# Kernel optimization log

Hardware: AMD Instinct MI355X
Metric: run time of the kernel (lower is better)

## Reference

```python
import jax, jax.numpy as jnp
import numpy as np

EMBED_DIM = 768
NUM_HEADS = 12
HEAD_DIM = EMBED_DIM // NUM_HEADS
SCALE = HEAD_DIM ** -0.5


def setup_inputs() -> dict:
    key = jax.random.key(0)
    ks = jax.random.split(key, 9)
    B, S, D = 2, 2048, EMBED_DIM
    init = 1.0 / np.sqrt(D)  # ~ nn.Linear default uniform scale
    x = jax.random.normal(ks[0], (B, S, D), dtype=jnp.float32)
    Wq = jax.random.uniform(ks[1], (D, D), jnp.float32, -init, init)
    bq = jax.random.uniform(ks[2], (D,), jnp.float32, -init, init)
    Wk = jax.random.uniform(ks[3], (D, D), jnp.float32, -init, init)
    bk = jax.random.uniform(ks[4], (D,), jnp.float32, -init, init)
    Wv = jax.random.uniform(ks[5], (D, D), jnp.float32, -init, init)
    bv = jax.random.uniform(ks[6], (D,), jnp.float32, -init, init)
    Wo = jax.random.uniform(ks[7], (D, D), jnp.float32, -init, init)
    bo = jax.random.uniform(ks[8], (D,), jnp.float32, -init, init)
    return {"x": x, "Wq": Wq, "bq": bq, "Wk": Wk, "bk": bk,
            "Wv": Wv, "bv": bv, "Wo": Wo, "bo": bo}


def reference(x, Wq, bq, Wk, bk, Wv, bv, Wo, bo):
    B, S, D = x.shape
    H, Dh = NUM_HEADS, HEAD_DIM
    # projections; weights stored as (in, out) so x @ W == torch Linear with W.T
    q = (x @ Wq + bq).reshape(B, S, H, Dh).transpose(0, 2, 1, 3)  # [B,H,S,Dh]
    k = (x @ Wk + bk).reshape(B, S, H, Dh).transpose(0, 2, 1, 3)
    v = (x @ Wv + bv).reshape(B, S, H, Dh).transpose(0, 2, 1, 3)
    scores = jnp.einsum("bhqd,bhkd->bhqk", q, k) * SCALE        # [B,H,S,S]
    weights = jax.nn.softmax(scores, axis=-1)
    out = jnp.einsum("bhqk,bhkd->bhqd", weights, v)              # [B,H,S,Dh]
    out = out.transpose(0, 2, 1, 3).reshape(B, S, D)
    return out @ Wo + bo
```

## Files before the change

kernel.cpp:

```cpp
#include <hip/hip_runtime.h>
#include <math.h>

#define BB 2
#define SS 2048
#define DDIM 768
#define HH 12
#define DH 64
#define NROWS (BB*SS)
#define NQT2 (SS/128)

typedef _Float16 f16;
typedef _Float16 half2v __attribute__((ext_vector_type(2)));
typedef __fp16 fp16x2 __attribute__((ext_vector_type(2)));
typedef _Float16 half4 __attribute__((ext_vector_type(4)));
typedef _Float16 half8 __attribute__((ext_vector_type(8)));
typedef float f32x4 __attribute__((ext_vector_type(4)));
typedef float f32x16 __attribute__((ext_vector_type(16)));
typedef unsigned int u32;
typedef unsigned int u32x4v __attribute__((ext_vector_type(4)));

__device__ __forceinline__ half2v cvt_pk_f16(float a, float b) {
    fp16x2 t = __builtin_amdgcn_cvt_pkrtz(a, b);
    return __builtin_bit_cast(half2v, t);
}

#define MFMA16(a,b,c) __builtin_amdgcn_mfma_f32_16x16x32_f16((a),(b),(c),0,0,0)
#define MFMA32(a,b,c) __builtin_amdgcn_mfma_f32_32x32x16_f16((a),(b),(c),0,0,0)
#define QSCALE (0.125f * 1.44269504088896f)
#define M_STATIC 10.0f

__device__ __forceinline__ int swz(int row, int chunk16) {
    return row*128 + ((chunk16 ^ (row & 7)) << 4);
}

__global__ __launch_bounds__(256) void prep_w(const float* __restrict__ Wq, const float* __restrict__ Wk,
                                              const float* __restrict__ Wv, const float* __restrict__ Wo,
                                              f16* __restrict__ Wt)
{
    const int z = blockIdx.z;
    const float* W = z==0 ? Wq : (z==1 ? Wk : (z==2 ? Wv : Wo));
    f16* out = Wt + (size_t)z * DDIM * DDIM;

    __shared__ float tile[64][65];
    const int t = threadIdx.x;
    const int k0 = blockIdx.x*64, n0 = blockIdx.y*64;

    const int kr = t >> 2, nc = (t & 3) * 16;
    #pragma unroll
    for (int i = 0; i < 4; ++i) {
        float4 v = *(const float4*)&W[(size_t)(k0+kr)*DDIM + n0 + nc + i*4];
        tile[kr][nc+i*4+0] = v.x; tile[kr][nc+i*4+1] = v.y;
        tile[kr][nc+i*4+2] = v.z; tile[kr][nc+i*4+3] = v.w;
    }
    __syncthreads();
    const int nr = t >> 2, kc = (t & 3) * 16;
    half8 h0, h1;
    #pragma unroll
    for (int j = 0; j < 8; ++j) {
        h0[j] = (f16)tile[kc + j][nr];
        h1[j] = (f16)tile[kc + 8 + j][nr];
    }
    *(half8*)&out[(size_t)(n0+nr)*DDIM + k0 + kc]     = h0;
    *(half8*)&out[(size_t)(n0+nr)*DDIM + k0 + kc + 8] = h1;
}

__global__ __launch_bounds__(256) void proj_qkv(const float* __restrict__ x, const f16* __restrict__ Wt,
        const float* __restrict__ bq, const float* __restrict__ bk, const float* __restrict__ bv,
        f16* __restrict__ qb, f16* __restrict__ kb2, f16* __restrict__ vtb)
{
    const int z = blockIdx.z;
    const f16* Wz = Wt + (size_t)z * DDIM * DDIM;
    const float* bias = z==0 ? bq : (z==1 ? bk : bv);
    const float qscale = (z==0) ? QSCALE : 1.0f;

    __shared__ __align__(16) unsigned char lds[64*1024];

    const int tid = threadIdx.x;
    const int l = tid & 63, w = tid >> 6;
    const int g = l >> 4, qi = l & 15;
    const int wm = w >> 1, wn = w & 1;
    const int m0 = blockIdx.x * 128, n0 = blockIdx.y * 128;

    f32x4 acc[4][4];
    #pragma unroll
    for (int i=0;i<4;i++)
        #pragma unroll
        for (int j=0;j<4;j++) { f32x4 zv = {0.f,0.f,0.f,0.f}; acc[i][j] = zv; }

    half8 sa[4], sb[4];

#define GLOAD(t) { \
        _Pragma("unroll") \
        for (int i = 0; i < 4; ++i) { \
            int c = i*256 + tid, row = c >> 3, kc = c & 7; \
            const float* xp = &x[(size_t)(m0+row)*DDIM + (t)*64 + kc*8]; \
            float4 a0 = *(const float4*)xp; \
            float4 a1 = *(const float4*)(xp + 4); \
            half8 hv = {(f16)a0.x,(f16)a0.y,(f16)a0.z,(f16)a0.w, \
                        (f16)a1.x,(f16)a1.y,(f16)a1.z,(f16)a1.w}; \
            sa[i] = hv; \
            sb[i] = *(const half8*)&Wz[(size_t)(n0+row)*DDIM + (t)*64 + kc*8]; \
        } }

#define GWRT(bufi) { \
        unsigned char* As_ = lds + (bufi)*32768; \
        unsigned char* Bs_ = As_ + 16384; \
        _Pragma("unroll") \
        for (int i = 0; i < 4; ++i) { \
            int c = i*256 + tid, row = c >> 3, kc = c & 7; \
            *(half8*)(As_ + swz(row, kc)) = sa[i]; \
            *(half8*)(Bs_ + swz(row, kc)) = sb[i]; \
        } }

    GLOAD(0); GWRT(0);
    __syncthreads();

    for (int t = 0; t < 12; ++t) {
        const int cur = t & 1;
        if (t < 11) GLOAD(t+1);

        const unsigned char* As = lds + cur*32768;
        const unsigned char* Bs = As + 16384;

        half8 af[4][2], bf[4][2];
        #pragma unroll
        for (int mt = 0; mt < 4; ++mt) {
            int row = wm*64 + mt*16 + qi;
            #pragma unroll
            for (int kh = 0; kh < 2; ++kh)
                af[mt][kh] = *(const half8*)(As + swz(row, kh*4 + g));
        }
        #pragma unroll
        for (int nt = 0; nt < 4; ++nt) {
            int row = wn*64 + nt*16 + qi;
            #pragma unroll
            for (int kh = 0; kh < 2; ++kh)
                bf[nt][kh] = *(const half8*)(Bs + swz(row, kh*4 + g));
        }
        __builtin_amdgcn_s_setprio(1);
        #pragma unroll
        for (int mt = 0; mt < 4; ++mt)
            #pragma unroll
            for (int nt = 0; nt < 4; ++nt) {
                acc[mt][nt] = MFMA16(af[mt][0], bf[nt][0], acc[mt][nt]);
                acc[mt][nt] = MFMA16(af[mt][1], bf[nt][1], acc[mt][nt]);
            }
        __builtin_amdgcn_s_setprio(0);

        if (t < 11) GWRT(cur^1);
        __syncthreads();
    }

    if (z == 2) {
        #pragma unroll
        for (int mt = 0; mt < 4; ++mt)
            #pragma unroll
            for (int nt = 0; nt < 4; ++nt) {
                int m = m0 + wm*64 + mt*16 + g*4;
                int n = n0 + wn*64 + nt*16 + qi;
                int b = m >> 11, s = m & 2047;
                int h = n >> 6,  d = n & 63;
                float bs = bias[n];
                half4 o4 = {(f16)(acc[mt][nt][0] + bs), (f16)(acc[mt][nt][1] + bs),
                            (f16)(acc[mt][nt][2] + bs), (f16)(acc[mt][nt][3] + bs)};
                *(half4*)&vtb[(((size_t)(b*HH + h))*DH + d)*SS + s] = o4;
            }
    } else {
        f16* out = (z == 0) ? qb : kb2;
        #pragma unroll
        for (int mt = 0; mt < 4; ++mt)
            #pragma unroll
            for (int nt = 0; nt < 4; ++nt)
                #pragma unroll
                for (int r = 0; r < 4; ++r) {
                    int m = m0 + wm*64 + mt*16 + g*4 + r;
                    int n = n0 + wn*64 + nt*16 + qi;
                    float v = (acc[mt][nt][r] + bias[n]) * qscale;
                    int b = m >> 11, s = m & 2047;
                    int h = n >> 6,  d = n & 63;
                    out[(((size_t)(b*HH + h))*SS + s)*DH + d] = (f16)v;
                }
    }
#undef GLOAD
#undef GWRT
}

__global__ __launch_bounds__(256) void attn_mfma(
        const f16* __restrict__ qbuf, const f16* __restrict__ kbuf,
        const f16* __restrict__ vtbuf, f16* __restrict__ pO, float* __restrict__ mlb)
{
    __shared__ __align__(16) unsigned char lds[32*1024];

    const int tid = threadIdx.x;
    const int l = tid & 63, w = tid >> 6;
    const int q31 = l & 31, hl = l >> 5;
    const int qt = blockIdx.x, h = blockIdx.y;
    const int b = blockIdx.z >> 1, khalf = blockIdx.z & 1;
    const int q0 = qt * 128 + w * 32;
    const size_t base = ((size_t)(b * HH + h)) * SS * DH;
    const int key0 = khalf * (SS/2);
    const int pid = (b * HH + h) * NQT2 + qt;

    half8 qf[4];
    #pragma unroll
    for (int s = 0; s < 4; ++s)
        qf[s] = *(const half8*)&qbuf[base + (size_t)(q0 + q31)*DH + s*16 + hl*8];

    f32x16 oacc[2];
    #pragma unroll
    for (int dt = 0; dt < 2; ++dt)
        #pragma unroll
        for (int i = 0; i < 16; ++i) oacc[dt][i] = 0.f;
    float lsum = 0.f;
    f32x16 minit16;
    #pragma unroll
    for (int i = 0; i < 16; ++i) minit16[i] = -M_STATIC;

    half8 sk[2], svv[2];

#define LOADT(t) { \
        _Pragma("unroll") \
        for (int i = 0; i < 2; ++i) { \
            int c = i*256 + tid, row = c >> 3, col = c & 7; \
            sk[i]  = *(const half8*)&kbuf[base + (size_t)(key0 + (t)*64 + row)*DH + col*8]; \
            svv[i] = *(const half8*)&vtbuf[base + (size_t)row*SS + key0 + (t)*64 + col*8]; \
        } }

#define WRT(bufi) { \
        unsigned char* Kw_ = lds + (bufi)*16384; \
        unsigned char* Vw_ = Kw_ + 8192; \
        _Pragma("unroll") \
        for (int i = 0; i < 2; ++i) { \
            int c = i*256 + tid, row = c >> 3, col = c & 7; \
            *(half8*)(Kw_ + swz(row, col)) = sk[i]; \
            *(half8*)(Vw_ + swz(row, col)) = svv[i]; \
        } }

    LOADT(0); WRT(0);
    __syncthreads();

    for (int t = 0; t < 16; ++t) {
        const int cur = t & 1;
        if (t < 15) LOADT(t+1);

        const unsigned char* Kb = lds + cur*16384;
        const unsigned char* Vb = Kb + 8192;

        half8 kA[2][4];
        #pragma unroll
        for (int mt = 0; mt < 2; ++mt)
            #pragma unroll
            for (int s = 0; s < 4; ++s)
                kA[mt][s] = *(const half8*)(Kb + swz(mt*32 + q31, 2*s + hl));
        half8 vA[2][4];
        #pragma unroll
        for (int dt = 0; dt < 2; ++dt)
            #pragma unroll
            for (int ks = 0; ks < 4; ++ks)
                vA[dt][ks] = *(const half8*)(Vb + swz(dt*32 + q31, 2*ks + hl));

        half2v ph[16];
        #pragma unroll
        for (int mt = 0; mt < 2; ++mt) {
            __builtin_amdgcn_s_setprio(1);
            f32x16 sv = minit16;
            #pragma unroll
            for (int s = 0; s < 4; ++s)
                sv = MFMA32(kA[mt][s], qf[s], sv);
            __builtin_amdgcn_s_setprio(0);
            #pragma unroll
            for (int r = 0; r < 16; r += 2)
                ph[mt*8 + (r>>1)] = cvt_pk_f16(exp2f(sv[r]), exp2f(sv[r+1]));
        }

        {
            half2v t01 = (ph[0]+ph[1]) + (ph[2]+ph[3]);
            half2v t23 = (ph[4]+ph[5]) + (ph[6]+ph[7]);
            half2v t45 = (ph[8]+ph[9]) + (ph[10]+ph[11]);
            half2v t67 = (ph[12]+ph[13]) + (ph[14]+ph[15]);
            half2v tt = (t01+t23) + (t45+t67);
            float rs = (float)tt[0] + (float)tt[1];
            rs += __shfl_xor(rs, 32);
            lsum += rs;
        }

        half8 pf[4];
        #pragma unroll
        for (int ks = 0; ks < 4; ++ks) {
            u32 x0 = __builtin_bit_cast(u32, ph[4*ks + 0]);
            u32 x2 = __builtin_bit_cast(u32, ph[4*ks + 2]);
            asm volatile("v_permlane32_swap_b32 %0, %1" : "+v"(x0), "+v"(x2));
            u32 x1 = __builtin_bit_cast(u32, ph[4*ks + 1]);
            u32 x3 = __builtin_bit_cast(u32, ph[4*ks + 3]);
            asm volatile("v_permlane32_swap_b32 %0, %1" : "+v"(x1), "+v"(x3));
            u32x4v tv = {x0, x1, x2, x3};
            pf[ks] = __builtin_bit_cast(half8, tv);
        }

        __builtin_amdgcn_s_setprio(1);
        #pragma unroll
        for (int dt = 0; dt < 2; ++dt)
            #pragma unroll
            for (int ks = 0; ks < 4; ++ks)
                oacc[dt] = MFMA32(vA[dt][ks], pf[ks], oacc[dt]);
        __builtin_amdgcn_s_setprio(0);

        if (t < 15) WRT(cur^1);
        __syncthreads();
    }

    f16* po = pO + ((size_t)pid*2 + khalf) * (128*64);
    float* mlp = mlb + ((size_t)pid*2 + khalf) * 128;
    const int qw = w*32 + q31;
    const float inv = 1.0f / lsum;
    #pragma unroll
    for (int dt = 0; dt < 2; ++dt)
        #pragma unroll
        for (int g2 = 0; g2 < 4; ++g2) {
            half4 o4 = {(f16)(oacc[dt][g2*4+0]*inv), (f16)(oacc[dt][g2*4+1]*inv),
                        (f16)(oacc[dt][g2*4+2]*inv), (f16)(oacc[dt][g2*4+3]*inv)};
            *(half4*)&po[qw*64 + dt*32 + g2*8 + hl*4] = o4;
        }
    if (hl == 0) mlp[qw] = lsum;
#undef LOADT
#undef WRT
}

__global__ __launch_bounds__(256) void proj_out(const f16* __restrict__ pO, const float* __restrict__ mlb,
                                                const f16* __restrict__ Wt, const float* __restrict__ bo,
                                                float* __restrict__ out)
{
    const f16* Wz = Wt + (size_t)3 * DDIM * DDIM;

    __shared__ __align__(16) unsigned char lds[64*1024];

    const int tid = threadIdx.x;
    const int l = tid & 63, w = tid >> 6;
    const int g = l >> 4, qi = l & 15;
    const int wm = w >> 1, wn = w & 1;
    const int m0 = blockIdx.x * 128, n0 = blockIdx.y * 128;

    f32x4 acc[4][4];
    #pragma unroll
    for (int i=0;i<4;i++)
        #pragma unroll
        for (int j=0;j<4;j++) { f32x4 zv = {0.f,0.f,0.f,0.f}; acc[i][j] = zv; }

    half8 sa[4], sb[4];

#define GLOAD(t) { \
        _Pragma("unroll") \
        for (int i = 0; i < 4; ++i) { \
            int c = i*256 + tid, row = c >> 3, kc = c & 7; \
            int m = m0 + row, bb_ = m >> 11, ss_ = m & 2047; \
            int qt_ = ss_ >> 7, qr_ = ss_ & 127; \
            int pid_ = (bb_*HH + (t))*NQT2 + qt_; \
            const f16* P0_ = pO + ((size_t)pid_*2 + 0)*(128*64) + qr_*64 + kc*8; \
            const f16* P1_ = pO + ((size_t)pid_*2 + 1)*(128*64) + qr_*64 + kc*8; \
            half8 xv = *(const half8*)P0_; \
            half8 yv = *(const half8*)P1_; \
            float l0 = mlb[((size_t)pid_*2 + 0)*128 + qr_]; \
            float l1 = mlb[((size_t)pid_*2 + 1)*128 + qr_]; \
            float winv = 1.0f / (l0 + l1); \
            float w0 = l0 * winv, w1 = l1 * winv; \
            half8 rv; \
            _Pragma("unroll") \
            for (int j = 0; j < 8; ++j) \
                rv[j] = (f16)(w0*(float)xv[j] + w1*(float)yv[j]); \
            sa[i] = rv; \
            sb[i] = *(const half8*)&Wz[(size_t)(n0+row)*DDIM + (t)*64 + kc*8]; \
        } }

#define GWRT(bufi) { \
        unsigned char* As_ = lds + (bufi)*32768; \
        unsigned char* Bs_ = As_ + 16384; \
        _Pragma("unroll") \
        for (int i = 0; i < 4; ++i) { \
            int c = i*256 + tid, row = c >> 3, kc = c & 7; \
            *(half8*)(As_ + swz(row, kc)) = sa[i]; \
            *(half8*)(Bs_ + swz(row, kc)) = sb[i]; \
        } }

    GLOAD(0); GWRT(0);
    __syncthreads();

    for (int t = 0; t < 12; ++t) {
        const int cur = t & 1;
        if (t < 11) GLOAD(t+1);

        const unsigned char* As = lds + cur*32768;
        const unsigned char* Bs = As + 16384;

        half8 af[4][2], bf[4][2];
        #pragma unroll
        for (int mt = 0; mt < 4; ++mt) {
            int row = wm*64 + mt*16 + qi;
            #pragma unroll
            for (int kh = 0; kh < 2; ++kh)
                af[mt][kh] = *(const half8*)(As + swz(row, kh*4 + g));
        }
        #pragma unroll
        for (int nt = 0; nt < 4; ++nt) {
            int row = wn*64 + nt*16 + qi;
            #pragma unroll
            for (int kh = 0; kh < 2; ++kh)
                bf[nt][kh] = *(const half8*)(Bs + swz(row, kh*4 + g));
        }
        __builtin_amdgcn_s_setprio(1);
        #pragma unroll
        for (int mt = 0; mt < 4; ++mt)
            #pragma unroll
            for (int nt = 0; nt < 4; ++nt) {
                acc[mt][nt] = MFMA16(af[mt][0], bf[nt][0], acc[mt][nt]);
                acc[mt][nt] = MFMA16(af[mt][1], bf[nt][1], acc[mt][nt]);
            }
        __builtin_amdgcn_s_setprio(0);

        if (t < 11) GWRT(cur^1);
        __syncthreads();
    }

    #pragma unroll
    for (int mt = 0; mt < 4; ++mt)
        #pragma unroll
        for (int nt = 0; nt < 4; ++nt)
            #pragma unroll
            for (int r = 0; r < 4; ++r) {
                int m = m0 + wm*64 + mt*16 + g*4 + r;
                int n = n0 + wn*64 + nt*16 + qi;
                out[(size_t)m*DDIM + n] = acc[mt][nt][r] + bo[n];
            }
#undef GLOAD
#undef GWRT
}

extern "C" void kernel_launch(void* const* d_in, const int* in_sizes, int n_in,
                              void* d_out, int out_size, void* d_ws, size_t ws_size,
                              hipStream_t stream)
{
    const float* x  = (const float*)d_in[0];
    const float* Wq = (const float*)d_in[1];
    const float* bq = (const float*)d_in[2];
    const float* Wk = (const float*)d_in[3];
    const float* bk = (const float*)d_in[4];
    const float* Wv = (const float*)d_in[5];
    const float* bv = (const float*)d_in[6];
    const float* Wo = (const float*)d_in[7];
    const float* bo = (const float*)d_in[8];

    char* ws = (char*)d_ws;
    const size_t WT_B  = (size_t)4 * DDIM * DDIM * 2;
    const size_t HB_B  = (size_t)BB * HH * SS * DH * 2;
    const size_t PO_B  = (size_t)BB * HH * NQT2 * 2 * 128 * 64 * 2;

    f16* Wt = (f16*)ws;
    f16* qb = (f16*)(ws + WT_B);
    f16* kb = (f16*)(ws + WT_B + HB_B);
    f16* vt = (f16*)(ws + WT_B + 2*HB_B);
    f16* pO = (f16*)(ws + WT_B + 3*HB_B);
    float* mlb = (float*)(ws + WT_B + 3*HB_B + PO_B);

    prep_w<<<dim3(DDIM/64, DDIM/64, 4), 256, 0, stream>>>(Wq, Wk, Wv, Wo, Wt);
    proj_qkv<<<dim3(NROWS/128, DDIM/128, 3), 256, 0, stream>>>(x, Wt, bq, bk, bv, qb, kb, vt);
    attn_mfma<<<dim3(NQT2, HH, BB*2), 256, 0, stream>>>(qb, kb, vt, pO, mlb);
    proj_out<<<dim3(NROWS/128, DDIM/128), 256, 0, stream>>>(pO, mlb, Wt, bo, (float*)d_out);
}
```

Before: 118.4 us.

## Split attention keys four ways and add a separate combine kernel

Splits the key range of each attention block into four parts instead of two, doubling the number of attention workgroups and halving each one's loop length. Partial outputs are merged by a new attn_combine kernel that writes a normalized per-head buffer, which proj_out now reads directly instead of merging two partials itself. This aims to raise parallelism and shorten per-block latency. In exchange it adds more partial-output memory traffic and an extra kernel launch.

```diff
diff --git a/kernel.cpp b/kernel.cpp
--- a/kernel.cpp
+++ b/kernel.cpp
@@ -8,6 +8,7 @@
 #define DH 64
 #define NROWS (BB*SS)
 #define NQT2 (SS/128)
+#define NSPLIT 4
 
 typedef _Float16 f16;
 typedef _Float16 half2v __attribute__((ext_vector_type(2)));
@@ -195,10 +196,10 @@
     const int l = tid & 63, w = tid >> 6;
     const int q31 = l & 31, hl = l >> 5;
     const int qt = blockIdx.x, h = blockIdx.y;
-    const int b = blockIdx.z >> 1, khalf = blockIdx.z & 1;
+    const int b = blockIdx.z >> 2, kq = blockIdx.z & 3;
     const int q0 = qt * 128 + w * 32;
     const size_t base = ((size_t)(b * HH + h)) * SS * DH;
-    const int key0 = khalf * (SS/2);
+    const int key0 = kq * (SS/NSPLIT);
     const int pid = (b * HH + h) * NQT2 + qt;
 
     half8 qf[4];
@@ -239,9 +240,9 @@
     LOADT(0); WRT(0);
     __syncthreads();
 
-    for (int t = 0; t < 16; ++t) {
+    for (int t = 0; t < 8; ++t) {
         const int cur = t & 1;
-        if (t < 15) LOADT(t+1);
+        if (t < 7) LOADT(t+1);
 
         const unsigned char* Kb = lds + cur*16384;
         const unsigned char* Vb = Kb + 8192;
@@ -305,12 +306,12 @@
                 oacc[dt] = MFMA32(vA[dt][ks], pf[ks], oacc[dt]);
         __builtin_amdgcn_s_setprio(0);
 
-        if (t < 15) WRT(cur^1);
+        if (t < 7) WRT(cur^1);
         __syncthreads();
     }
 
-    f16* po = pO + ((size_t)pid*2 + khalf) * (128*64);
-    float* mlp = mlb + ((size_t)pid*2 + khalf) * 128;
+    f16* po = pO + ((size_t)pid*NSPLIT + kq) * (128*64);
+    float* mlp = mlb + ((size_t)pid*NSPLIT + kq) * 128;
     const int qw = w*32 + q31;
     const float inv = 1.0f / lsum;
     #pragma unroll
@@ -326,9 +327,46 @@
 #undef WRT
 }
 
-__global__ __launch_bounds__(256) void proj_out(const f16* __restrict__ pO, const float* __restrict__ mlb,
-                                                const f16* __restrict__ Wt, const float* __restrict__ bo,
-                                                float* __restrict__ out)
+__global__ __launch_bounds__(256) void attn_combine(
+        const f16* __restrict__ pO, const float* __restrict__ mlb, f16* __restrict__ ob)
+{
+    const int gr = blockIdx.x*64 + (threadIdx.x >> 2);
+    const int dg = (threadIdx.x & 3) << 4;
+    const int bh = gr >> 11, s = gr & 2047;
+    const int qt = s >> 7, qr = s & 127;
+    const int pid = bh * NQT2 + qt;
+
+    float lv[NSPLIT], lt = 0.f;
+    #pragma unroll
+    for (int i = 0; i < NSPLIT; ++i) {
+        lv[i] = mlb[((size_t)pid*NSPLIT + i)*128 + qr];
+        lt += lv[i];
+    }
+    const float inv = 1.0f / lt;
+
+    float a0[8] = {}, a1[8] = {};
+    #pragma unroll
+    for (int i = 0; i < NSPLIT; ++i) {
+        const f16* Oi = pO + ((size_t)pid*NSPLIT + i)*(128*64) + qr*64 + dg;
+        half8 x0 = *(const half8*)Oi;
+        half8 x1 = *(const half8*)(Oi + 8);
+        float wi = lv[i] * inv;
+        #pragma unroll
+        for (int j = 0; j < 8; ++j) {
+            a0[j] += wi * (float)x0[j];
+            a1[j] += wi * (float)x1[j];
+        }
+    }
+    half8 r0, r1;
+    #pragma unroll
+    for (int j = 0; j < 8; ++j) { r0[j] = (f16)a0[j]; r1[j] = (f16)a1[j]; }
+    f16* dst = &ob[((size_t)bh*SS + s)*DH + dg];
+    *(half8*)dst = r0;
+    *(half8*)(dst + 8) = r1;
+}
+
+__global__ __launch_bounds__(256) void proj_out(const f16* __restrict__ obuf, const f16* __restrict__ Wt,
+                                                const float* __restrict__ bo, float* __restrict__ out)
 {
     const f16* Wz = Wt + (size_t)3 * DDIM * DDIM;
 
@@ -353,21 +391,7 @@
         for (int i = 0; i < 4; ++i) { \
             int c = i*256 + tid, row = c >> 3, kc = c & 7; \
             int m = m0 + row, bb_ = m >> 11, ss_ = m & 2047; \
-            int qt_ = ss_ >> 7, qr_ = ss_ & 127; \
-            int pid_ = (bb_*HH + (t))*NQT2 + qt_; \
-            const f16* P0_ = pO + ((size_t)pid_*2 + 0)*(128*64) + qr_*64 + kc*8; \
-            const f16* P1_ = pO + ((size_t)pid_*2 + 1)*(128*64) + qr_*64 + kc*8; \
-            half8 xv = *(const half8*)P0_; \
-            half8 yv = *(const half8*)P1_; \
-            float l0 = mlb[((size_t)pid_*2 + 0)*128 + qr_]; \
-            float l1 = mlb[((size_t)pid_*2 + 1)*128 + qr_]; \
-            float winv = 1.0f / (l0 + l1); \
-            float w0 = l0 * winv, w1 = l1 * winv; \
-            half8 rv; \
-            _Pragma("unroll") \
-            for (int j = 0; j < 8; ++j) \
-                rv[j] = (f16)(w0*(float)xv[j] + w1*(float)yv[j]); \
-            sa[i] = rv; \
+            sa[i] = *(const half8*)&obuf[(((size_t)(bb_*HH + (t)))*SS + ss_)*DH + kc*8]; \
             sb[i] = *(const half8*)&Wz[(size_t)(n0+row)*DDIM + (t)*64 + kc*8]; \
         } }
 
@@ -451,7 +475,8 @@
     char* ws = (char*)d_ws;
     const size_t WT_B  = (size_t)4 * DDIM * DDIM * 2;
     const size_t HB_B  = (size_t)BB * HH * SS * DH * 2;
-    const size_t PO_B  = (size_t)BB * HH * NQT2 * 2 * 128 * 64 * 2;
+    const size_t PO_B  = (size_t)BB * HH * NQT2 * NSPLIT * 128 * 64 * 2;
+    const size_t ML_B  = (size_t)BB * HH * NQT2 * NSPLIT * 128 * 4;
 
     f16* Wt = (f16*)ws;
     f16* qb = (f16*)(ws + WT_B);
@@ -459,9 +484,11 @@
     f16* vt = (f16*)(ws + WT_B + 2*HB_B);
     f16* pO = (f16*)(ws + WT_B + 3*HB_B);
     float* mlb = (float*)(ws + WT_B + 3*HB_B + PO_B);
+    f16* ob = (f16*)(ws + WT_B + 3*HB_B + PO_B + ML_B);
 
     prep_w<<<dim3(DDIM/64, DDIM/64, 4), 256, 0, stream>>>(Wq, Wk, Wv, Wo, Wt);
     proj_qkv<<<dim3(NROWS/128, DDIM/128, 3), 256, 0, stream>>>(x, Wt, bq, bk, bv, qb, kb, vt);
-    attn_mfma<<<dim3(NQT2, HH, BB*2), 256, 0, stream>>>(qb, kb, vt, pO, mlb);
-    proj_out<<<dim3(NROWS/128, DDIM/128), 256, 0, stream>>>(pO, mlb, Wt, bo, (float*)d_out);
-}
+    attn_mfma<<<dim3(NQT2, HH, BB*NSPLIT), 256, 0, stream>>>(qb, kb, vt, pO, mlb);
+    attn_combine<<<dim3(BB*HH*SS/64), 256, 0, stream>>>(pO, mlb, ob);
+    proj_out<<<dim3(NROWS/128, DDIM/128), 256, 0, stream>>>(ob, Wt, bo, (float*)d_out);
+}
```

Result: no change. 118.6 us (+0.2%).
